# Optimization experiments

Hardware: AMD Instinct MI355X
Metric: run time of the kernel (lower is better)

Reference implementation:

```python
import jax, jax.numpy as jnp
import numpy as np

SR = 44100        # sample rate (init kwarg)
WINDOWS = 2048    # fft window size (init kwarg)
B, P = 128, 192   # batch, number of peaking filters


def setup_inputs() -> dict:
    key = jax.random.key(0)
    k1, k2, k3 = jax.random.split(key, 3)
    # center frequencies in (40 Hz, 0.45*sr), gains in dB, quality factors in [0.5, 2)
    center = jax.random.uniform(k1, (B, P), minval=40.0, maxval=0.45 * SR, dtype=jnp.float32)
    gain = 6.0 * jax.random.normal(k2, (B, P), dtype=jnp.float32)
    q = jax.random.uniform(k3, (B, P), minval=0.5, maxval=2.0, dtype=jnp.float32)
    return {"center": center, "gain": gain, "q": q}


def _biquad(a, b, windows):
    # a, b: [..., 3] filter taps; rfft zero-pads to `windows` samples.
    iir = jnp.fft.rfft(a, n=windows, axis=-1)  # [..., windows//2+1] complex
    fir = jnp.fft.rfft(b, n=windows, axis=-1)
    return fir / iir


def reference(center, gain, q):
    """Peaking equalizer: [..., windows//2+1] complex frequency response."""
    w0 = (2.0 * np.pi / SR) * center
    A = jnp.exp(gain * (np.log(10.0) / 40.0))
    alpha = jnp.sin(w0) / 2.0 / q
    cos_w0 = jnp.cos(w0)
    b0 = 1.0 + alpha * A
    b1 = -2.0 * cos_w0
    b2 = 1.0 - alpha * A
    a0 = 1.0 + alpha / A
    a1 = -2.0 * cos_w0
    a2 = 1.0 - alpha / A
    return _biquad(jnp.stack([a0, a1, a2], axis=-1),
                   jnp.stack([b0, b1, b2], axis=-1), WINDOWS)
```

## Files before the change

kernel.cpp:

```cpp
#include <hip/hip_runtime.h>
#include <math.h>

constexpr int NBINS = 1025;
constexpr int NROWS = 128 * 192;
constexpr int RPB   = 16;
constexpr int NBLK  = NROWS / RPB;
constexpr int DWB   = RPB * NBINS;
constexpr int QPB   = DWB / 4;

__device__ inline unsigned int f2bf(float f) {
    unsigned int u = __float_as_uint(f);
    return (u + 0x7FFFu + ((u >> 16) & 1u)) >> 16;
}

__global__ __launch_bounds__(256) void eq_kernel(
    const float* __restrict__ center,
    const float* __restrict__ gain,
    const float* __restrict__ q,
    unsigned int* __restrict__ out)
{
    __shared__ float2 tab[NBINS];
    __shared__ float4 rp[RPB];

    const int tid = threadIdx.x;
    if (tid < RPB) {
        const int row = blockIdx.x * RPB + tid;
        float w0 = 1.4247585730565955e-4f * center[row];
        float sh, ch;
        sincosf(0.5f * w0, &sh, &ch);
        float A = exp2f(0.08304820237218406f * gain[row]);
        float alpha = sh * ch / q[row];
        float g2 = alpha / A;
        rp[tid] = make_float4(sh, alpha * alpha, g2, alpha * A - g2);
    }
    for (int k = tid; k < NBINS; k += 256) {
        float st, ct;
        sincosf((float)k * 1.5339807878856412e-3f, &st, &ct);
        tab[k] = make_float2(st, ct);
    }
    __syncthreads();

    uint4* __restrict__ ob = (uint4*)(out + (size_t)blockIdx.x * DWB);
    for (int g = tid; g < QPB; g += 256) {
        const int f0 = 4 * g;
        unsigned int w[4];
        #pragma unroll
        for (int j = 0; j < 4; ++j) {
            const int f = f0 + j;
            const int r = f / NBINS;
            const int k = f - r * NBINS;
            const float4 P = rp[r];
            const float2 t = tab[k];
            float d  = 2.0f * (P.x - t.x) * (P.x + t.x);
            float s  = 2.0f * t.x * t.y;
            float d2 = d * d;
            float g2s = P.z * s;
            float den = fmaf(g2s, g2s, d2);
            float inv = __builtin_amdgcn_rcpf(den);
            float re = fmaf(P.y, s * s, d2) * inv;
            float im = P.w * s * d * inv;
            w[j] = f2bf(im) | (f2bf(re) << 16);
        }
        ob[g] = make_uint4(w[0], w[1], w[2], w[3]);
    }
}

extern "C" void kernel_launch(void* const* d_in, const int* in_sizes, int n_in,
                              void* d_out, int out_size, void* d_ws, size_t ws_size,
                              hipStream_t stream) {
    const float* center = (const float*)d_in[0];
    const float* gain   = (const float*)d_in[1];
    const float* q      = (const float*)d_in[2];
    eq_kernel<<<NBLK, 256, 0, stream>>>(center, gain, q, (unsigned int*)d_out);
}
```

Before: 115.3 us.

## Restructure per-wave row mapping, fold constants, and special-case the Nyquist bin

Each wave now handles four full rows, with lanes striding over bins. This removes the per-element division/modulo by NBINS and the repeated row-parameter lookup. The algebra is rescaled so the table stores sin and sin(2θ) and the row parameters carry the 0.25 and 0.5 factors, which saves multiplies per bin. The Nyquist bin (k=1024) is written as a constant (re=1, im=0) by a single thread per row. The cost is losing the 16-byte vector stores: rows are 1025 words long, so the coalesced 4-byte stores are misaligned relative to 16B.

```diff
diff --git a/kernel.cpp b/kernel.cpp
--- a/kernel.cpp
+++ b/kernel.cpp
@@ -5,8 +5,6 @@
 constexpr int NROWS = 128 * 192;
 constexpr int RPB   = 16;
 constexpr int NBLK  = NROWS / RPB;
-constexpr int DWB   = RPB * NBINS;
-constexpr int QPB   = DWB / 4;
 
 __device__ inline unsigned int f2bf(float f) {
     unsigned int u = __float_as_uint(f);
@@ -19,10 +17,13 @@
     const float* __restrict__ q,
     unsigned int* __restrict__ out)
 {
-    __shared__ float2 tab[NBINS];
+    __shared__ float2 tab[1024];
     __shared__ float4 rp[RPB];
 
-    const int tid = threadIdx.x;
+    const int tid  = threadIdx.x;
+    const int wave = tid >> 6;
+    const int lane = tid & 63;
+
     if (tid < RPB) {
         const int row = blockIdx.x * RPB + tid;
         float w0 = 1.4247585730565955e-4f * center[row];
@@ -31,38 +32,39 @@
         float A = exp2f(0.08304820237218406f * gain[row]);
         float alpha = sh * ch / q[row];
         float g2 = alpha / A;
-        rp[tid] = make_float4(sh, alpha * alpha, g2, alpha * A - g2);
+        float gd = alpha * A - g2;
+        rp[tid] = make_float4(sh, 0.25f * alpha * alpha, 0.25f * g2 * g2, 0.5f * gd);
     }
-    for (int k = tid; k < NBINS; k += 256) {
+    for (int k = tid; k < 1024; k += 256) {
         float st, ct;
         sincosf((float)k * 1.5339807878856412e-3f, &st, &ct);
-        tab[k] = make_float2(st, ct);
+        tab[k] = make_float2(st, 2.0f * st * ct);
     }
     __syncthreads();
 
-    uint4* __restrict__ ob = (uint4*)(out + (size_t)blockIdx.x * DWB);
-    for (int g = tid; g < QPB; g += 256) {
-        const int f0 = 4 * g;
-        unsigned int w[4];
+    const int rbase = blockIdx.x * RPB + wave * 4;
+    for (int j = 0; j < 4; ++j) {
+        const int row = rbase + j;
+        const float4 P = rp[wave * 4 + j];
+        unsigned int* __restrict__ orow = out + (size_t)row * NBINS;
         #pragma unroll
-        for (int j = 0; j < 4; ++j) {
-            const int f = f0 + j;
-            const int r = f / NBINS;
-            const int k = f - r * NBINS;
-            const float4 P = rp[r];
+        for (int i = 0; i < 16; ++i) {
+            const int k = lane + (i << 6);
             const float2 t = tab[k];
-            float d  = 2.0f * (P.x - t.x) * (P.x + t.x);
-            float s  = 2.0f * t.x * t.y;
-            float d2 = d * d;
-            float g2s = P.z * s;
-            float den = fmaf(g2s, g2s, d2);
+            float u  = P.x - t.x;
+            float v  = P.x + t.x;
+            float dp = u * v;
+            float D2 = dp * dp;
+            float S2 = t.y * t.y;
+            float den = fmaf(P.z, S2, D2);
             float inv = __builtin_amdgcn_rcpf(den);
-            float re = fmaf(P.y, s * s, d2) * inv;
-            float im = P.w * s * d * inv;
-            w[j] = f2bf(im) | (f2bf(re) << 16);
+            float re = fmaf(P.y, S2, D2) * inv;
+            float im = P.w * t.y * dp * inv;
+            orow[k] = f2bf(im) | (f2bf(re) << 16);
         }
-        ob[g] = make_uint4(w[0], w[1], w[2], w[3]);
     }
+    if (tid < RPB)
+        out[(size_t)(blockIdx.x * RPB + tid) * NBINS + 1024] = 0x3F800000u;
 }
 
 extern "C" void kernel_launch(void* const* d_in, const int* in_sizes, int n_in,
```

New measurement: 112.4 us. 2.5% less time.
